# Optimization experiments

Hardware: AMD Instinct MI355X
Metric: run time of the kernel (lower is better)

Reference implementation:

```python
import jax, jax.numpy as jnp
import numpy as np

N_LIG, N_TGT, E = 100000, 20000, 250000
LIG_IN, TGT_IN, H = 4, 1280, 128


def setup_inputs() -> dict:
    key = jax.random.key(0)
    ks = jax.random.split(key, 12)
    def lin_w(k, fan_in, fan_out):
        # kaiming-uniform-ish init, stored as [in, out] for x @ W
        bound = 1.0 / np.sqrt(fan_in)
        return jax.random.uniform(k, (fan_in, fan_out), jnp.float32, -bound, bound)
    return {
        "x_ligand": jax.random.normal(ks[0], (N_LIG, LIG_IN), jnp.float32),
        "x_target": jax.random.normal(ks[1], (N_TGT, TGT_IN), jnp.float32),
        "edge_src": jax.random.randint(ks[2], (E,), 0, N_LIG, jnp.int32),
        "edge_dst": jax.random.randint(ks[3], (E,), 0, N_TGT, jnp.int32),
        # SAGEConv (ligand -> target): lin_l on aggregated ligand msgs, lin_r on target self
        "W_lt_l": lin_w(ks[4], LIG_IN, H),
        "b_lt_l": jnp.zeros((H,), jnp.float32),
        "W_lt_r": lin_w(ks[5], TGT_IN, H),
        # SAGEConv (target -> ligand): lin_l on aggregated target msgs, lin_r on ligand self
        "W_tl_l": lin_w(ks[6], TGT_IN, H),
        "b_tl_l": jnp.zeros((H,), jnp.float32),
        "W_tl_r": lin_w(ks[7], LIG_IN, H),
        # edge predictor: Linear(2H -> 1)
        "W_ep": lin_w(ks[8], 2 * H, 1),
        "b_ep": jnp.zeros((1,), jnp.float32),
    }


def _mean_agg(x_src, src_idx, dst_idx, num_dst):
    # gather per-edge source features, scatter-mean onto destination nodes
    msg = x_src[src_idx]                                             # [E, F]
    s = jax.ops.segment_sum(msg, dst_idx, num_segments=num_dst)      # [N_dst, F]
    cnt = jax.ops.segment_sum(jnp.ones((src_idx.shape[0], 1), x_src.dtype),
                              dst_idx, num_segments=num_dst)         # [N_dst, 1]
    return s / jnp.maximum(cnt, 1.0)


def reference(x_ligand, x_target, edge_src, edge_dst,
              W_lt_l, b_lt_l, W_lt_r, W_tl_l, b_tl_l, W_tl_r, W_ep, b_ep):
    # SAGEConv (ligand, binds_to, target): aggregate ligand msgs into targets
    agg_t = _mean_agg(x_ligand, edge_src, edge_dst, N_TGT)           # [N_TGT, LIG_IN]
    t_out = agg_t @ W_lt_l + b_lt_l + x_target @ W_lt_r              # [N_TGT, H]
    # SAGEConv (target, binds_to, ligand): reversed edges (flip(0))
    agg_l = _mean_agg(x_target, edge_dst, edge_src, N_LIG)           # [N_LIG, TGT_IN]
    l_out = agg_l @ W_tl_l + b_tl_l + x_ligand @ W_tl_r              # [N_LIG, H]
    l_out = jax.nn.relu(l_out)
    t_out = jax.nn.relu(t_out)
    # edge predictor: gather endpoints, concat, linear, squeeze
    edge_feats = jnp.concatenate([l_out[edge_src], t_out[edge_dst]], axis=-1)  # [E, 2H]
    out = (edge_feats @ W_ep + b_ep).squeeze(-1)                     # [E]
    return out
```

## Files before the change

kernel.cpp:

```cpp
#include <hip/hip_runtime.h>
#include <hip/hip_bf16.h>


#define H 128
#define K_DIM 1280
#define LIG_IN 4
#define CAP_L 24
#define CAP_T 48

typedef __attribute__((ext_vector_type(8))) short bf16x8;
typedef __attribute__((ext_vector_type(4))) float f32x4;

#define AS1(p) ((const __attribute__((address_space(1))) void*)(p))
#define AS3(p) ((__attribute__((address_space(3))) void*)(p))

__global__ void fill_both(const int* __restrict__ src, const int* __restrict__ dst,
                          int* __restrict__ cur_l, int* __restrict__ cur_t,
                          int* __restrict__ adjd, int* __restrict__ adjs, int E)
{
    int e = blockIdx.x * blockDim.x + threadIdx.x;
    if (e >= E) return;
    int s = src[e], d = dst[e];
    int p = atomicAdd(&cur_l[s], 1);
    adjd[s * CAP_L + p] = d;
    int q = atomicAdd(&cur_t[d], 1);
    adjs[d * CAP_T + q] = s;
}

__global__ void cast_wt(const float* __restrict__ Wl, const float* __restrict__ Wr,
                        __hip_bfloat16* __restrict__ Wt, int n)
{
    int idx = blockIdx.x * blockDim.x + threadIdx.x;
    if (idx >= n) return;
    int nr = idx / K_DIM, k = idx - nr * K_DIM;
    float v = (nr < H) ? Wl[k * H + nr] : Wr[k * H + (nr - H)];
    Wt[idx] = __float2bfloat16(v);
}

__device__ inline bf16x8 cvt8(float4 u, float4 v)
{
    union { __hip_bfloat16 h[8]; bf16x8 f; } r;
    r.h[0] = __float2bfloat16(u.x); r.h[1] = __float2bfloat16(u.y);
    r.h[2] = __float2bfloat16(u.z); r.h[3] = __float2bfloat16(u.w);
    r.h[4] = __float2bfloat16(v.x); r.h[5] = __float2bfloat16(v.y);
    r.h[6] = __float2bfloat16(v.z); r.h[7] = __float2bfloat16(v.w);
    return r.f;
}

#define NCHUNK 10
__global__ __launch_bounds__(256, 2)
void gemm_fused(const float* __restrict__ Xf,
                const unsigned short* __restrict__ Wt,
                float* __restrict__ y_tl, float* __restrict__ t_lin, int M)
{
    __shared__ short Bs[2][128 * 128];

    const int t = threadIdx.x;
    const int w = t >> 6, lane = t & 63;
    const int m = lane & 15, q = lane >> 4;
    const int mb = blockIdx.x >> 1, nb = blockIdx.x & 1;
    const int bm = mb * 64;
    const int nb128 = nb * 128;

    const int rowc = min(bm + w * 16 + m, M - 1);
    const float* gA = Xf + (size_t)rowc * K_DIM + q * 8;

    int bn[8], bcc[8], bdst[8];
#pragma unroll
    for (int i = 0; i < 8; ++i) {
        int L = i * 256 + t;
        bn[i] = L >> 4;
        int cp = L & 15;
        bcc[i] = cp ^ (bn[i] & 15);
        bdst[i] = (i * 256 + w * 64) * 16;
    }

    f32x4 acc[8];
#pragma unroll
    for (int j = 0; j < 8; ++j) acc[j] = (f32x4){0.f, 0.f, 0.f, 0.f};

    float4 a4[2][8];

#pragma unroll
    for (int s = 0; s < 4; ++s) {
        a4[0][2 * s]     = *(const float4*)(gA + s * 32);
        a4[0][2 * s + 1] = *(const float4*)(gA + s * 32 + 4);
    }
#pragma unroll
    for (int i = 0; i < 8; ++i)
        __builtin_amdgcn_global_load_lds(AS1(Wt + (size_t)(nb128 + bn[i]) * K_DIM + bcc[i] * 8),
                                         AS3((char*)Bs[0] + bdst[i]), 16, 0, 0);
    __syncthreads();

#pragma unroll
    for (int c = 0; c < NCHUNK; ++c) {
        const int cur = c & 1, nxt = cur ^ 1;
        if (c + 1 < NCHUNK) {
            const int kc = (c + 1) * 128;
#pragma unroll
            for (int i = 0; i < 8; ++i)
                __builtin_amdgcn_global_load_lds(
                    AS1(Wt + (size_t)(nb128 + bn[i]) * K_DIM + kc + bcc[i] * 8),
                    AS3((char*)Bs[nxt] + bdst[i]), 16, 0, 0);
#pragma unroll
            for (int s = 0; s < 4; ++s) {
                a4[nxt][2 * s]     = *(const float4*)(gA + kc + s * 32);
                a4[nxt][2 * s + 1] = *(const float4*)(gA + kc + s * 32 + 4);
            }
        }
#pragma unroll
        for (int s = 0; s < 4; ++s) {
            bf16x8 aF = cvt8(a4[cur][2 * s], a4[cur][2 * s + 1]);
#pragma unroll
            for (int j = 0; j < 8; ++j) {
                bf16x8 bF = *(const bf16x8*)((const char*)Bs[cur] +
                              (j * 16 + m) * 256 + (((s * 4 + q) ^ m) * 16));
                acc[j] = __builtin_amdgcn_mfma_f32_16x16x32_bf16(aF, bF, acc[j], 0, 0, 0);
            }
        }
        __syncthreads();
    }

    float* __restrict__ Y = nb ? t_lin : y_tl;
#pragma unroll
    for (int j = 0; j < 8; ++j) {
        int col = j * 16 + m;
#pragma unroll
        for (int r = 0; r < 4; ++r) {
            int row = bm + w * 16 + q * 4 + r;
            if (row < M) Y[(size_t)row * H + col] = acc[j][r];
        }
    }
}

__global__ void target_post(const int* __restrict__ cur_t, const int* __restrict__ adjs,
                            const float* __restrict__ xl, const float* __restrict__ t_lin,
                            const float* __restrict__ W_lt_l, const float* __restrict__ b_lt_l,
                            const float* __restrict__ W_ep,
                            float* __restrict__ st, int NT)
{
    int wid = (blockIdx.x * blockDim.x + threadIdx.x) >> 6;
    int lane = threadIdx.x & 63;
    if (wid >= NT) return;
    int cnt = cur_t[wid];
    float a0 = 0.f, a1 = 0.f, a2 = 0.f, a3 = 0.f;
    for (int j = lane; j < cnt; j += 64) {
        int s = adjs[wid * CAP_T + j];
        float4 v = *(const float4*)(xl + (size_t)s * LIG_IN);
        a0 += v.x; a1 += v.y; a2 += v.z; a3 += v.w;
    }
#pragma unroll
    for (int off = 32; off > 0; off >>= 1) {
        a0 += __shfl_xor(a0, off);
        a1 += __shfl_xor(a1, off);
        a2 += __shfl_xor(a2, off);
        a3 += __shfl_xor(a3, off);
    }
    float inv = 1.0f / fmaxf((float)cnt, 1.0f);
    a0 *= inv; a1 *= inv; a2 *= inv; a3 *= inv;
    float acc = 0.f;
#pragma unroll
    for (int p = 0; p < 2; ++p) {
        int h = lane + p * 64;
        float v = a0 * W_lt_l[h] + a1 * W_lt_l[H + h] + a2 * W_lt_l[2 * H + h] +
                  a3 * W_lt_l[3 * H + h] + b_lt_l[h] + t_lin[(size_t)wid * H + h];
        v = fmaxf(v, 0.f);
        acc += v * W_ep[H + h];
    }
#pragma unroll
    for (int off = 32; off > 0; off >>= 1) acc += __shfl_down(acc, off);
    if (lane == 0) st[wid] = acc;
}

__global__ void ligand_gather_post(const int* __restrict__ cur_l, const int* __restrict__ adjd,
                                   const float* __restrict__ y_tl,
                                   const float* __restrict__ xl,
                                   const float* __restrict__ W_tl_r, const float* __restrict__ b_tl_l,
                                   const float* __restrict__ W_ep,
                                   float* __restrict__ sl, int NL)
{
    int wid = (blockIdx.x * blockDim.x + threadIdx.x) >> 6;
    int lane = threadIdx.x & 63;
    if (wid >= NL) return;
    int cnt = cur_l[wid];
    float a0 = 0.f, a1 = 0.f;
    for (int j = 0; j < cnt; ++j) {
        int d = adjd[wid * CAP_L + j];
        float2 f = ((const float2*)(y_tl + (size_t)d * H))[lane];
        a0 += f.x;
        a1 += f.y;
    }
    float inv = 1.0f / fmaxf((float)cnt, 1.0f);
    float4 x = *(const float4*)(xl + (size_t)wid * LIG_IN);
    float acc = 0.f;
    {
        int h = 2 * lane;
        float v = a0 * inv + b_tl_l[h] +
                  x.x * W_tl_r[h] + x.y * W_tl_r[H + h] +
                  x.z * W_tl_r[2 * H + h] + x.w * W_tl_r[3 * H + h];
        v = fmaxf(v, 0.f);
        acc += v * W_ep[h];
    }
    {
        int h = 2 * lane + 1;
        float v = a1 * inv + b_tl_l[h] +
                  x.x * W_tl_r[h] + x.y * W_tl_r[H + h] +
                  x.z * W_tl_r[2 * H + h] + x.w * W_tl_r[3 * H + h];
        v = fmaxf(v, 0.f);
        acc += v * W_ep[h];
    }
#pragma unroll
    for (int off = 32; off > 0; off >>= 1) acc += __shfl_down(acc, off);
    if (lane == 0) sl[wid] = acc;
}

__global__ void edge_out(const int* __restrict__ src, const int* __restrict__ dst,
                         const float* __restrict__ sl, const float* __restrict__ st,
                         const float* __restrict__ b_ep, float* __restrict__ out, int E)
{
    int e = blockIdx.x * blockDim.x + threadIdx.x;
    if (e >= E) return;
    out[e] = sl[src[e]] + st[dst[e]] + b_ep[0];
}

extern "C" void kernel_launch(void* const* d_in, const int* in_sizes, int n_in,
                              void* d_out, int out_size, void* d_ws, size_t ws_size,
                              hipStream_t stream) {
    const float* x_ligand = (const float*)d_in[0];
    const float* x_target = (const float*)d_in[1];
    const int*   edge_src = (const int*)d_in[2];
    const int*   edge_dst = (const int*)d_in[3];
    const float* W_lt_l   = (const float*)d_in[4];
    const float* b_lt_l   = (const float*)d_in[5];
    const float* W_lt_r   = (const float*)d_in[6];
    const float* W_tl_l   = (const float*)d_in[7];
    const float* b_tl_l   = (const float*)d_in[8];
    const float* W_tl_r   = (const float*)d_in[9];
    const float* W_ep     = (const float*)d_in[10];
    const float* b_ep     = (const float*)d_in[11];
    float* out = (float*)d_out;

    const int NL = in_sizes[0] / LIG_IN;
    const int NT = in_sizes[1] / K_DIM;
    const int E  = in_sizes[2];

    char* ws = (char*)d_ws;
    size_t off = 0;
    auto take = [&](size_t bytes) { size_t o = off; off += (bytes + 15) & ~(size_t)15; return o; };
    size_t off_Wt     = take((size_t)2 * H * K_DIM * 2);
    size_t off_y_tl   = take((size_t)NT * H * 4);
    size_t off_t_lin  = take((size_t)NT * H * 4);
    size_t off_adjd   = take((size_t)NL * CAP_L * 4);
    size_t off_adjs   = take((size_t)NT * CAP_T * 4);
    size_t off_cur_l  = take((size_t)NL * 4);
    size_t off_cur_t  = take((size_t)NT * 4);
    size_t off_sl     = take((size_t)NL * 4);
    size_t off_st     = take((size_t)NT * 4);
    if (off > ws_size) {
        hipMemsetAsync(d_out, 0, (size_t)out_size * 4, stream);
        return;
    }

    __hip_bfloat16* Wt = (__hip_bfloat16*)(ws + off_Wt);
    float* y_tl  = (float*)(ws + off_y_tl);
    float* t_lin = (float*)(ws + off_t_lin);
    int*   adjd  = (int*)(ws + off_adjd);
    int*   adjs  = (int*)(ws + off_adjs);
    int*   cur_l = (int*)(ws + off_cur_l);
    int*   cur_t = (int*)(ws + off_cur_t);
    float* sl    = (float*)(ws + off_sl);
    float* st    = (float*)(ws + off_st);

    hipMemsetAsync(cur_l, 0, off_sl - off_cur_l, stream);

    int nw = 2 * H * K_DIM;
    cast_wt<<<(nw + 255) / 256, 256, 0, stream>>>(W_tl_l, W_lt_r, Wt, nw);

    gemm_fused<<<((NT + 63) / 64) * 2, 256, 0, stream>>>(x_target, (const unsigned short*)Wt,
                                                         y_tl, t_lin, NT);

    fill_both<<<(E + 255) / 256, 256, 0, stream>>>(edge_src, edge_dst,
                                                   cur_l, cur_t, adjd, adjs, E);

    target_post<<<(NT * 64 + 255) / 256, 256, 0, stream>>>(cur_t, adjs, x_ligand, t_lin,
                                                           W_lt_l, b_lt_l, W_ep, st, NT);
    ligand_gather_post<<<(NL * 64 + 255) / 256, 256, 0, stream>>>(cur_l, adjd, y_tl, x_ligand,
                                                                  W_tl_r, b_tl_l, W_ep, sl, NL);
    edge_out<<<(E + 255) / 256, 256, 0, stream>>>(edge_src, edge_dst, sl, st, b_ep, out, E);
}
```

Before: 306.6 us.

## Retile GEMM to 32-row blocks with LDS-staged A and single-buffered B

The fused x_target GEMM moves from 64-row tiles with per-wave direct A loads and a double-buffered B tile to 32-row tiles. A is staged through padded LDS with a two-chunk register prefetch, and each wave computes a 32x32 sub-tile over a single-buffered B. The smaller shared footprint and the launch bound raised to 3 are meant to raise occupancy and double the number of blocks. The cost is an extra barrier per chunk, B loads no longer overlapping compute, and the loss of the M-bound clamp and row guard, which assumes NT is divisible by 32.

Result: slower. 366.5 us (+19.6%).

```diff
diff --git a/kernel.cpp b/kernel.cpp
--- a/kernel.cpp
+++ b/kernel.cpp
@@ -48,22 +48,27 @@
 }
 
 #define NCHUNK 10
-__global__ __launch_bounds__(256, 2)
+#define AROW 132
+__global__ __launch_bounds__(256, 3)
 void gemm_fused(const float* __restrict__ Xf,
                 const unsigned short* __restrict__ Wt,
                 float* __restrict__ y_tl, float* __restrict__ t_lin, int M)
 {
-    __shared__ short Bs[2][128 * 128];
+    __shared__ float As[32 * AROW];
+    __shared__ short Bs[128 * 128];
 
     const int t = threadIdx.x;
     const int w = t >> 6, lane = t & 63;
     const int m = lane & 15, q = lane >> 4;
     const int mb = blockIdx.x >> 1, nb = blockIdx.x & 1;
-    const int bm = mb * 64;
+    const int bm = mb * 32;
     const int nb128 = nb * 128;
 
-    const int rowc = min(bm + w * 16 + m, M - 1);
-    const float* gA = Xf + (size_t)rowc * K_DIM + q * 8;
+    const int ar = t >> 5;
+    const int ac = (t & 31) * 4;
+    const float* gA = Xf + (size_t)(bm + ar) * K_DIM + ac;
+
+    const int aw_base = ar * AROW + ac;
 
     int bn[8], bcc[8], bdst[8];
 #pragma unroll
@@ -75,60 +80,97 @@
         bdst[i] = (i * 256 + w * 64) * 16;
     }
 
-    f32x4 acc[8];
-#pragma unroll
-    for (int j = 0; j < 8; ++j) acc[j] = (f32x4){0.f, 0.f, 0.f, 0.f};
-
-    float4 a4[2][8];
-
-#pragma unroll
-    for (int s = 0; s < 4; ++s) {
-        a4[0][2 * s]     = *(const float4*)(gA + s * 32);
-        a4[0][2 * s + 1] = *(const float4*)(gA + s * 32 + 4);
-    }
+    f32x4 acc[2][2];
+#pragma unroll
+    for (int i = 0; i < 2; ++i)
+#pragma unroll
+        for (int j = 0; j < 2; ++j)
+            acc[i][j] = (f32x4){0.f, 0.f, 0.f, 0.f};
+
+    float4 ar0[4], ar1[4];
+
+#pragma unroll
+    for (int s = 0; s < 4; ++s)
+        ar0[s] = *(const float4*)(gA + (size_t)s * 8 * K_DIM);
 #pragma unroll
     for (int i = 0; i < 8; ++i)
         __builtin_amdgcn_global_load_lds(AS1(Wt + (size_t)(nb128 + bn[i]) * K_DIM + bcc[i] * 8),
-                                         AS3((char*)Bs[0] + bdst[i]), 16, 0, 0);
+                                         AS3((char*)Bs + bdst[i]), 16, 0, 0);
+#pragma unroll
+    for (int s = 0; s < 4; ++s)
+        *(float4*)(As + aw_base + s * 8 * AROW) = ar0[s];
+#pragma unroll
+    for (int s = 0; s < 4; ++s)
+        ar1[s] = *(const float4*)(gA + 128 + (size_t)s * 8 * K_DIM);
     __syncthreads();
 
 #pragma unroll
     for (int c = 0; c < NCHUNK; ++c) {
-        const int cur = c & 1, nxt = cur ^ 1;
+        if (c + 2 < NCHUNK) {
+            const int kc2 = (c + 2) * 128;
+            if ((c & 1) == 0) {
+#pragma unroll
+                for (int s = 0; s < 4; ++s)
+                    ar0[s] = *(const float4*)(gA + kc2 + (size_t)s * 8 * K_DIM);
+            } else {
+#pragma unroll
+                for (int s = 0; s < 4; ++s)
+                    ar1[s] = *(const float4*)(gA + kc2 + (size_t)s * 8 * K_DIM);
+            }
+        }
+#pragma unroll
+        for (int ks = 0; ks < 4; ++ks) {
+            bf16x8 aF[2], bF[2];
+#pragma unroll
+            for (int i = 0; i < 2; ++i) {
+                const float* ap = As + (m + 16 * i) * AROW + ks * 32 + q * 8;
+                float4 u = *(const float4*)ap;
+                float4 v = *(const float4*)(ap + 4);
+                aF[i] = cvt8(u, v);
+            }
+#pragma unroll
+            for (int j = 0; j < 2; ++j) {
+                int n_loc = w * 32 + j * 16 + m;
+                bF[j] = *(const bf16x8*)((const char*)Bs + n_loc * 256 + (((ks * 4 + q) ^ m) * 16));
+            }
+#pragma unroll
+            for (int i = 0; i < 2; ++i)
+#pragma unroll
+                for (int j = 0; j < 2; ++j)
+                    acc[i][j] = __builtin_amdgcn_mfma_f32_16x16x32_bf16(aF[i], bF[j], acc[i][j], 0, 0, 0);
+        }
+        __syncthreads();
         if (c + 1 < NCHUNK) {
+            if ((c & 1) == 0) {
+#pragma unroll
+                for (int s = 0; s < 4; ++s)
+                    *(float4*)(As + aw_base + s * 8 * AROW) = ar1[s];
+            } else {
+#pragma unroll
+                for (int s = 0; s < 4; ++s)
+                    *(float4*)(As + aw_base + s * 8 * AROW) = ar0[s];
+            }
             const int kc = (c + 1) * 128;
 #pragma unroll
             for (int i = 0; i < 8; ++i)
                 __builtin_amdgcn_global_load_lds(
                     AS1(Wt + (size_t)(nb128 + bn[i]) * K_DIM + kc + bcc[i] * 8),
-                    AS3((char*)Bs[nxt] + bdst[i]), 16, 0, 0);
-#pragma unroll
-            for (int s = 0; s < 4; ++s) {
-                a4[nxt][2 * s]     = *(const float4*)(gA + kc + s * 32);
-                a4[nxt][2 * s + 1] = *(const float4*)(gA + kc + s * 32 + 4);
-            }
+                    AS3((char*)Bs + bdst[i]), 16, 0, 0);
+            __syncthreads();
         }
-#pragma unroll
-        for (int s = 0; s < 4; ++s) {
-            bf16x8 aF = cvt8(a4[cur][2 * s], a4[cur][2 * s + 1]);
-#pragma unroll
-            for (int j = 0; j < 8; ++j) {
-                bf16x8 bF = *(const bf16x8*)((const char*)Bs[cur] +
-                              (j * 16 + m) * 256 + (((s * 4 + q) ^ m) * 16));
-                acc[j] = __builtin_amdgcn_mfma_f32_16x16x32_bf16(aF, bF, acc[j], 0, 0, 0);
-            }
-        }
-        __syncthreads();
     }
 
     float* __restrict__ Y = nb ? t_lin : y_tl;
 #pragma unroll
-    for (int j = 0; j < 8; ++j) {
-        int col = j * 16 + m;
-#pragma unroll
-        for (int r = 0; r < 4; ++r) {
-            int row = bm + w * 16 + q * 4 + r;
-            if (row < M) Y[(size_t)row * H + col] = acc[j][r];
+    for (int i = 0; i < 2; ++i) {
+#pragma unroll
+        for (int j = 0; j < 2; ++j) {
+            int col = w * 32 + j * 16 + m;
+#pragma unroll
+            for (int r = 0; r < 4; ++r) {
+                int row = bm + i * 16 + q * 4 + r;
+                Y[(size_t)row * H + col] = acc[i][j][r];
+            }
         }
     }
 }
@@ -276,8 +318,8 @@
     int nw = 2 * H * K_DIM;
     cast_wt<<<(nw + 255) / 256, 256, 0, stream>>>(W_tl_l, W_lt_r, Wt, nw);
 
-    gemm_fused<<<((NT + 63) / 64) * 2, 256, 0, stream>>>(x_target, (const unsigned short*)Wt,
-                                                         y_tl, t_lin, NT);
+    gemm_fused<<<(NT / 32) * 2, 256, 0, stream>>>(x_target, (const unsigned short*)Wt,
+                                                  y_tl, t_lin, NT);
 
     fill_both<<<(E + 255) / 256, 256, 0, stream>>>(edge_src, edge_dst,
                                                    cur_l, cur_t, adjd, adjs, E);
```

## Pre-swizzle weights into MFMA fragment order and drop LDS staging in GEMM

Applied to the files above, without the earlier changes.

The weight cast kernel now writes the bf16 weights in the exact per-lane MFMA fragment order, so the GEMM can load B fragments straight from global memory into registers. This removes the LDS double buffer, the async global-to-LDS copies and the per-chunk barriers. Each wave now computes 32 rows instead of 16, so every B fragment feeds two MFMAs, and the grid is halved. In exchange, B traffic now goes through L2/L1 per wave instead of being shared through LDS, and register pressure rises, with the launch-bounds occupancy hint removed.

Result: slower. 356.9 us (+16.4%).

```diff
diff --git a/kernel.cpp b/kernel.cpp
--- a/kernel.cpp
+++ b/kernel.cpp
@@ -7,12 +7,10 @@
 #define LIG_IN 4
 #define CAP_L 24
 #define CAP_T 48
+#define NSTEP 40
 
 typedef __attribute__((ext_vector_type(8))) short bf16x8;
 typedef __attribute__((ext_vector_type(4))) float f32x4;
-
-#define AS1(p) ((const __attribute__((address_space(1))) void*)(p))
-#define AS3(p) ((__attribute__((address_space(3))) void*)(p))
 
 __global__ void fill_both(const int* __restrict__ src, const int* __restrict__ dst,
                           int* __restrict__ cur_l, int* __restrict__ cur_t,
@@ -28,13 +26,15 @@
 }
 
 __global__ void cast_wt(const float* __restrict__ Wl, const float* __restrict__ Wr,
-                        __hip_bfloat16* __restrict__ Wt, int n)
+                        __hip_bfloat16* __restrict__ Wf, int total)
 {
     int idx = blockIdx.x * blockDim.x + threadIdx.x;
-    if (idx >= n) return;
-    int nr = idx / K_DIM, k = idx - nr * K_DIM;
-    float v = (nr < H) ? Wl[k * H + nr] : Wr[k * H + (nr - H)];
-    Wt[idx] = __float2bfloat16(v);
+    if (idx >= total) return;
+    int n = idx / K_DIM, k = idx - n * K_DIM;
+    float v = (n < H) ? Wl[k * H + n] : Wr[k * H + (n - H)];
+    int jt = n >> 4, m = n & 15;
+    int s = k >> 5, q = (k >> 3) & 3, e = k & 7;
+    Wf[(size_t)(((jt * NSTEP + s) * 64) + q * 16 + m) * 8 + e] = __float2bfloat16(v);
 }
 
 __device__ inline bf16x8 cvt8(float4 u, float4 v)
@@ -47,88 +47,76 @@
     return r.f;
 }
 
-#define NCHUNK 10
-__global__ __launch_bounds__(256, 2)
+__global__ __launch_bounds__(256)
 void gemm_fused(const float* __restrict__ Xf,
-                const unsigned short* __restrict__ Wt,
+                const unsigned short* __restrict__ Wf,
                 float* __restrict__ y_tl, float* __restrict__ t_lin, int M)
 {
-    __shared__ short Bs[2][128 * 128];
-
     const int t = threadIdx.x;
     const int w = t >> 6, lane = t & 63;
     const int m = lane & 15, q = lane >> 4;
     const int mb = blockIdx.x >> 1, nb = blockIdx.x & 1;
-    const int bm = mb * 64;
-    const int nb128 = nb * 128;
-
-    const int rowc = min(bm + w * 16 + m, M - 1);
-    const float* gA = Xf + (size_t)rowc * K_DIM + q * 8;
-
-    int bn[8], bcc[8], bdst[8];
-#pragma unroll
-    for (int i = 0; i < 8; ++i) {
-        int L = i * 256 + t;
-        bn[i] = L >> 4;
-        int cp = L & 15;
-        bcc[i] = cp ^ (bn[i] & 15);
-        bdst[i] = (i * 256 + w * 64) * 16;
-    }
-
-    f32x4 acc[8];
-#pragma unroll
-    for (int j = 0; j < 8; ++j) acc[j] = (f32x4){0.f, 0.f, 0.f, 0.f};
-
-    float4 a4[2][8];
-
-#pragma unroll
-    for (int s = 0; s < 4; ++s) {
-        a4[0][2 * s]     = *(const float4*)(gA + s * 32);
-        a4[0][2 * s + 1] = *(const float4*)(gA + s * 32 + 4);
-    }
-#pragma unroll
-    for (int i = 0; i < 8; ++i)
-        __builtin_amdgcn_global_load_lds(AS1(Wt + (size_t)(nb128 + bn[i]) * K_DIM + bcc[i] * 8),
-                                         AS3((char*)Bs[0] + bdst[i]), 16, 0, 0);
-    __syncthreads();
-
-#pragma unroll
-    for (int c = 0; c < NCHUNK; ++c) {
-        const int cur = c & 1, nxt = cur ^ 1;
-        if (c + 1 < NCHUNK) {
-            const int kc = (c + 1) * 128;
-#pragma unroll
-            for (int i = 0; i < 8; ++i)
-                __builtin_amdgcn_global_load_lds(
-                    AS1(Wt + (size_t)(nb128 + bn[i]) * K_DIM + kc + bcc[i] * 8),
-                    AS3((char*)Bs[nxt] + bdst[i]), 16, 0, 0);
-#pragma unroll
-            for (int s = 0; s < 4; ++s) {
-                a4[nxt][2 * s]     = *(const float4*)(gA + kc + s * 32);
-                a4[nxt][2 * s + 1] = *(const float4*)(gA + kc + s * 32 + 4);
+    const int bm = mb * 128;
+    const int wrow = bm + w * 32;
+
+    const int r0 = min(wrow + m, M - 1);
+    const int r1 = min(wrow + 16 + m, M - 1);
+    const float* gA0 = Xf + (size_t)r0 * K_DIM + q * 8;
+    const float* gA1 = Xf + (size_t)r1 * K_DIM + q * 8;
+
+    const unsigned short* gB = Wf + (size_t)((nb * 8) * NSTEP * 64 + lane) * 8;
+
+    f32x4 acc[2][8];
+#pragma unroll
+    for (int i = 0; i < 2; ++i)
+#pragma unroll
+        for (int j = 0; j < 8; ++j)
+            acc[i][j] = (f32x4){0.f, 0.f, 0.f, 0.f};
+
+    float4 aA[2][2][2];
+    bf16x8 bB[2][8];
+
+    aA[0][0][0] = *(const float4*)(gA0);
+    aA[0][0][1] = *(const float4*)(gA0 + 4);
+    aA[0][1][0] = *(const float4*)(gA1);
+    aA[0][1][1] = *(const float4*)(gA1 + 4);
+#pragma unroll
+    for (int j = 0; j < 8; ++j)
+        bB[0][j] = *(const bf16x8*)(gB + (size_t)(j * NSTEP) * 64 * 8);
+
+#pragma unroll
+    for (int s = 0; s < NSTEP; ++s) {
+        const int cur = s & 1, nxt = cur ^ 1;
+        if (s + 1 < NSTEP) {
+            const int k1 = (s + 1) * 32;
+            aA[nxt][0][0] = *(const float4*)(gA0 + k1);
+            aA[nxt][0][1] = *(const float4*)(gA0 + k1 + 4);
+            aA[nxt][1][0] = *(const float4*)(gA1 + k1);
+            aA[nxt][1][1] = *(const float4*)(gA1 + k1 + 4);
+#pragma unroll
+            for (int j = 0; j < 8; ++j)
+                bB[nxt][j] = *(const bf16x8*)(gB + (size_t)(j * NSTEP + s + 1) * 64 * 8);
+        }
+        bf16x8 aF0 = cvt8(aA[cur][0][0], aA[cur][0][1]);
+        bf16x8 aF1 = cvt8(aA[cur][1][0], aA[cur][1][1]);
+#pragma unroll
+        for (int j = 0; j < 8; ++j) {
+            acc[0][j] = __builtin_amdgcn_mfma_f32_16x16x32_bf16(aF0, bB[cur][j], acc[0][j], 0, 0, 0);
+            acc[1][j] = __builtin_amdgcn_mfma_f32_16x16x32_bf16(aF1, bB[cur][j], acc[1][j], 0, 0, 0);
+        }
+    }
+
+    float* __restrict__ Y = nb ? t_lin : y_tl;
+#pragma unroll
+    for (int i = 0; i < 2; ++i) {
+#pragma unroll
+        for (int j = 0; j < 8; ++j) {
+            int col = j * 16 + m;
+#pragma unroll
+            for (int r = 0; r < 4; ++r) {
+                int row = wrow + i * 16 + q * 4 + r;
+                if (row < M) Y[(size_t)row * H + col] = acc[i][j][r];
             }
-        }
-#pragma unroll
-        for (int s = 0; s < 4; ++s) {
-            bf16x8 aF = cvt8(a4[cur][2 * s], a4[cur][2 * s + 1]);
-#pragma unroll
-            for (int j = 0; j < 8; ++j) {
-                bf16x8 bF = *(const bf16x8*)((const char*)Bs[cur] +
-                              (j * 16 + m) * 256 + (((s * 4 + q) ^ m) * 16));
-                acc[j] = __builtin_amdgcn_mfma_f32_16x16x32_bf16(aF, bF, acc[j], 0, 0, 0);
-            }
-        }
-        __syncthreads();
-    }
-
-    float* __restrict__ Y = nb ? t_lin : y_tl;
-#pragma unroll
-    for (int j = 0; j < 8; ++j) {
-        int col = j * 16 + m;
-#pragma unroll
-        for (int r = 0; r < 4; ++r) {
-            int row = bm + w * 16 + q * 4 + r;
-            if (row < M) Y[(size_t)row * H + col] = acc[j][r];
         }
     }
 }
@@ -276,8 +264,8 @@
     int nw = 2 * H * K_DIM;
     cast_wt<<<(nw + 255) / 256, 256, 0, stream>>>(W_tl_l, W_lt_r, Wt, nw);
 
-    gemm_fused<<<((NT + 63) / 64) * 2, 256, 0, stream>>>(x_target, (const unsigned short*)Wt,
-                                                         y_tl, t_lin, NT);
+    gemm_fused<<<((NT + 127) / 128) * 2, 256, 0, stream>>>(x_target, (const unsigned short*)Wt,
+                                                           y_tl, t_lin, NT);
 
     fill_both<<<(E + 255) / 256, 256, 0, stream>>>(edge_src, edge_dst,
                                                    cur_l, cur_t, adjd, adjs, E);
```

## Stage A tile in LDS and use 2x2 warp tiling with single-buffered K=64 chunks

Applied to the files above, without the earlier changes.

The fused GEMM now loads the fp32 A tile into swizzled shared memory through direct global-to-LDS loads, where before each warp read it into registers. Warps are arranged 2x2, each computing 32x64 outputs. This lets each A fragment be reused across 4 B fragments and each B fragment across 2 A fragments. The K loop now uses 20 single-buffered chunks of 64 with a sync before and after each load, which drops the double-buffered prefetch overlap. The launch_bounds occupancy hint is removed and LDS use per block falls, which may allow more blocks per CU.

New measurement: 297.5 us. 2.9% less time.

```diff
diff --git a/kernel.cpp b/kernel.cpp
--- a/kernel.cpp
+++ b/kernel.cpp
@@ -7,6 +7,7 @@
 #define LIG_IN 4
 #define CAP_L 24
 #define CAP_T 48
+#define NCH 20
 
 typedef __attribute__((ext_vector_type(8))) short bf16x8;
 typedef __attribute__((ext_vector_type(4))) float f32x4;
@@ -47,88 +48,109 @@
     return r.f;
 }
 
-#define NCHUNK 10
-__global__ __launch_bounds__(256, 2)
+__global__ __launch_bounds__(256)
 void gemm_fused(const float* __restrict__ Xf,
                 const unsigned short* __restrict__ Wt,
                 float* __restrict__ y_tl, float* __restrict__ t_lin, int M)
 {
-    __shared__ short Bs[2][128 * 128];
+    __shared__ float As[64 * 64];
+    __shared__ short Bs[128 * 64];
 
     const int t = threadIdx.x;
     const int w = t >> 6, lane = t & 63;
-    const int m = lane & 15, q = lane >> 4;
+    const int m16 = lane & 15, q = lane >> 4;
+    const int wm = w & 1, wn = w >> 1;
     const int mb = blockIdx.x >> 1, nb = blockIdx.x & 1;
     const int bm = mb * 64;
     const int nb128 = nb * 128;
 
-    const int rowc = min(bm + w * 16 + m, M - 1);
-    const float* gA = Xf + (size_t)rowc * K_DIM + q * 8;
-
-    int bn[8], bcc[8], bdst[8];
-#pragma unroll
-    for (int i = 0; i < 8; ++i) {
-        int L = i * 256 + t;
-        bn[i] = L >> 4;
-        int cp = L & 15;
-        bcc[i] = cp ^ (bn[i] & 15);
-        bdst[i] = (i * 256 + w * 64) * 16;
-    }
-
-    f32x4 acc[8];
-#pragma unroll
-    for (int j = 0; j < 8; ++j) acc[j] = (f32x4){0.f, 0.f, 0.f, 0.f};
-
-    float4 a4[2][8];
-
-#pragma unroll
-    for (int s = 0; s < 4; ++s) {
-        a4[0][2 * s]     = *(const float4*)(gA + s * 32);
-        a4[0][2 * s + 1] = *(const float4*)(gA + s * 32 + 4);
-    }
-#pragma unroll
-    for (int i = 0; i < 8; ++i)
-        __builtin_amdgcn_global_load_lds(AS1(Wt + (size_t)(nb128 + bn[i]) * K_DIM + bcc[i] * 8),
-                                         AS3((char*)Bs[0] + bdst[i]), 16, 0, 0);
+    const float* a_g[4];
+#pragma unroll
+    for (int i = 0; i < 4; ++i) {
+        int slot = i * 256 + w * 64 + lane;
+        int m = slot >> 4, cl = slot & 15;
+        int cg = cl ^ (m & 15);
+        int row = min(bm + m, M - 1);
+        a_g[i] = Xf + (size_t)row * K_DIM + cg * 4;
+    }
+    const unsigned short* b_g[4];
+#pragma unroll
+    for (int i = 0; i < 4; ++i) {
+        int slot = i * 256 + w * 64 + lane;
+        int n = slot >> 3, cl = slot & 7;
+        int cg = cl ^ (n & 7);
+        b_g[i] = Wt + (size_t)(nb128 + n) * K_DIM + cg * 8;
+    }
+
+    f32x4 acc[2][4];
+#pragma unroll
+    for (int i = 0; i < 2; ++i)
+#pragma unroll
+        for (int j = 0; j < 4; ++j)
+            acc[i][j] = (f32x4){0.f, 0.f, 0.f, 0.f};
+
+#pragma unroll
+    for (int i = 0; i < 4; ++i)
+        __builtin_amdgcn_global_load_lds(AS1(a_g[i]), AS3((char*)As + (i * 256 + w * 64) * 16), 16, 0, 0);
+#pragma unroll
+    for (int i = 0; i < 4; ++i)
+        __builtin_amdgcn_global_load_lds(AS1(b_g[i]), AS3((char*)Bs + (i * 256 + w * 64) * 16), 16, 0, 0);
     __syncthreads();
 
-#pragma unroll
-    for (int c = 0; c < NCHUNK; ++c) {
-        const int cur = c & 1, nxt = cur ^ 1;
-        if (c + 1 < NCHUNK) {
-            const int kc = (c + 1) * 128;
-#pragma unroll
-            for (int i = 0; i < 8; ++i)
-                __builtin_amdgcn_global_load_lds(
-                    AS1(Wt + (size_t)(nb128 + bn[i]) * K_DIM + kc + bcc[i] * 8),
-                    AS3((char*)Bs[nxt] + bdst[i]), 16, 0, 0);
-#pragma unroll
-            for (int s = 0; s < 4; ++s) {
-                a4[nxt][2 * s]     = *(const float4*)(gA + kc + s * 32);
-                a4[nxt][2 * s + 1] = *(const float4*)(gA + kc + s * 32 + 4);
+    for (int ch = 0; ch < NCH; ++ch) {
+#pragma unroll
+        for (int ks = 0; ks < 2; ++ks) {
+            bf16x8 aF[2];
+#pragma unroll
+            for (int i = 0; i < 2; ++i) {
+                int row = wm * 32 + i * 16 + m16;
+                int c = ks * 8 + q * 2;
+                int s0 = row * 16 + (c ^ m16);
+                int s1 = s0 ^ 1;
+                float4 u = *(const float4*)((const char*)As + s0 * 16);
+                float4 v = *(const float4*)((const char*)As + s1 * 16);
+                aF[i] = cvt8(u, v);
             }
-        }
-#pragma unroll
-        for (int s = 0; s < 4; ++s) {
-            bf16x8 aF = cvt8(a4[cur][2 * s], a4[cur][2 * s + 1]);
-#pragma unroll
-            for (int j = 0; j < 8; ++j) {
-                bf16x8 bF = *(const bf16x8*)((const char*)Bs[cur] +
-                              (j * 16 + m) * 256 + (((s * 4 + q) ^ m) * 16));
-                acc[j] = __builtin_amdgcn_mfma_f32_16x16x32_bf16(aF, bF, acc[j], 0, 0, 0);
+            bf16x8 bF[4];
+#pragma unroll
+            for (int j = 0; j < 4; ++j) {
+                int n = wn * 64 + j * 16 + m16;
+                int c = ks * 4 + q;
+                int s = n * 8 + (c ^ (n & 7));
+                bF[j] = *(const bf16x8*)((const char*)Bs + s * 16);
             }
+#pragma unroll
+            for (int i = 0; i < 2; ++i)
+#pragma unroll
+                for (int j = 0; j < 4; ++j)
+                    acc[i][j] = __builtin_amdgcn_mfma_f32_16x16x32_bf16(aF[i], bF[j], acc[i][j], 0, 0, 0);
         }
         __syncthreads();
+        if (ch + 1 < NCH) {
+            const int kc = (ch + 1) * 64;
+#pragma unroll
+            for (int i = 0; i < 4; ++i)
+                __builtin_amdgcn_global_load_lds(AS1(a_g[i] + kc),
+                                                 AS3((char*)As + (i * 256 + w * 64) * 16), 16, 0, 0);
+#pragma unroll
+            for (int i = 0; i < 4; ++i)
+                __builtin_amdgcn_global_load_lds(AS1(b_g[i] + kc),
+                                                 AS3((char*)Bs + (i * 256 + w * 64) * 16), 16, 0, 0);
+            __syncthreads();
+        }
     }
 
     float* __restrict__ Y = nb ? t_lin : y_tl;
 #pragma unroll
-    for (int j = 0; j < 8; ++j) {
-        int col = j * 16 + m;
-#pragma unroll
-        for (int r = 0; r < 4; ++r) {
-            int row = bm + w * 16 + q * 4 + r;
-            if (row < M) Y[(size_t)row * H + col] = acc[j][r];
+    for (int i = 0; i < 2; ++i) {
+#pragma unroll
+        for (int j = 0; j < 4; ++j) {
+            int col = wn * 64 + j * 16 + m16;
+#pragma unroll
+            for (int r = 0; r < 4; ++r) {
+                int row = bm + wm * 32 + i * 16 + q * 4 + r;
+                if (row < M) Y[(size_t)row * H + col] = acc[i][j][r];
+            }
         }
     }
 }
```
